# Kernel optimization log

Measured on AMD Instinct MI355X. Metric: run time of the kernel, lower is better.

## Reference

```python
import jax, jax.numpy as jnp
from jax import lax
import numpy as np


def _dw_xcorr_single(f, k):
    # f: (ch, Hf, Wf) search features; k: (ch, Hk, Wk) template kernel
    # Depthwise cross-correlation: one 2D correlation per channel.
    ch = f.shape[0]
    out = lax.conv_general_dilated(
        f[None],                 # (1, ch, Hf, Wf)
        k[:, None],              # (ch, 1, Hk, Wk) OIHW depthwise kernel
        window_strides=(1, 1),
        padding='VALID',
        dimension_numbers=('NCHW', 'OIHW', 'NCHW'),
        feature_group_count=ch,
    )
    return out[0]  # (ch, H, W)


def _conv3x3(x, w, b):
    # x: (N, C, H, W), w: (O, C, 3, 3), b: (O,)
    y = lax.conv_general_dilated(
        x, w, window_strides=(1, 1), padding='VALID',
        dimension_numbers=('NCHW', 'OIHW', 'NCHW'))
    return y + b[None, :, None, None]


def setup_inputs() -> dict:
    key = jax.random.key(0)
    k1, k2, k3, k4, k5, k6 = jax.random.split(key, 6)
    N, C = 128, 256
    x_f = jax.random.normal(k1, (N, C, 31, 31), dtype=jnp.float32)
    z_f = jax.random.normal(k2, (N, C, 7, 7), dtype=jnp.float32)
    # Conv params (Kaiming-uniform-like scale)
    s3 = 1.0 / np.sqrt(C * 9)
    heat_w = jax.random.uniform(k3, (1, C, 3, 3), jnp.float32, -s3, s3)
    heat_b = jax.random.uniform(k4, (1,), jnp.float32, -s3, s3)
    reg_w = jax.random.uniform(k5, (4, C, 3, 3), jnp.float32, -s3, s3)
    reg_b = jax.random.uniform(k6, (4,), jnp.float32, -s3, s3)
    return {"x_f": x_f, "z_f": z_f, "heat_w": heat_w, "heat_b": heat_b,
            "reg_w": reg_w, "reg_b": reg_b}


def reference(x_f, z_f, heat_w, heat_b, reg_w, reg_b):
    # Depthwise cross-correlation over batch (groups = N*ch in the original)
    corr = jax.vmap(_dw_xcorr_single)(x_f, z_f)  # (N, C, 25, 25)
    pred_heat = _conv3x3(corr, heat_w, heat_b)   # (N, 1, 23, 23)
    pred_reg = _conv3x3(corr, reg_w, reg_b)      # (N, 4, 23, 23)
    return (pred_heat, pred_reg)
```

## Files before the change

### kernel.cpp

```cpp
#include <hip/hip_runtime.h>

#define NB 128
#define NC 256
#define HX 31
#define WX 31
#define HC 25
#define WC 25
#define HO 23
#define WO 23
#define CHUNKS 8
#define CPB (NC / CHUNKS)
#define GRP 10
#define ZCH 56
#define WCH 48
#define CCH (HC * WC)

#define HEAT_SZ (NB * HO * WO)
#define REG_SZ  (NB * 4 * HO * WO)
#define OUT_TOTAL (HEAT_SZ + REG_SZ)

typedef float f4v __attribute__((ext_vector_type(4), aligned(4)));

__global__ void init_out_kernel(float* __restrict__ out,
                                const float* __restrict__ heat_b,
                                const float* __restrict__ reg_b) {
    int i = blockIdx.x * 256 + threadIdx.x;
    if (i >= OUT_TOTAL) return;
    if (i < HEAT_SZ) {
        out[i] = heat_b[0];
    } else {
        int j = i - HEAT_SZ;
        int o = (j / (HO * WO)) & 3;
        out[i] = reg_b[o];
    }
}

__launch_bounds__(256, 4)
__global__ void fused_head_kernel(const float* __restrict__ xf,
                                  const float* __restrict__ zf,
                                  const float* __restrict__ hw,
                                  const float* __restrict__ rw,
                                  float* __restrict__ out) {
    __shared__ __align__(16) float cs[GRP * CCH];
    __shared__ __align__(16) float zs[GRP * ZCH];
    __shared__ __align__(16) float ws[CPB * WCH];

    const int tid = threadIdx.x;
    const int n = blockIdx.x >> 3;
    const int chunk = blockIdx.x & 7;
    const int cbase = chunk * CPB;

    const int cl = tid / 25;
    const int tt = tid % 25;
    const int tr = tt / 5, tc = tt % 5;
    const int i0 = tr * 5, j0 = tc * 5;

    const int p0 = tid;
    const int p1 = tid + 256;
    const int p2 = tid + 512;
    const int oy0 = p0 / 23, ox0 = p0 - oy0 * 23;
    const int oy1 = p1 / 23, ox1 = p1 - oy1 * 23;
    const int oy2 = p2 / 23, ox2 = p2 - oy2 * 23;
    const int off0 = oy0 * WC + ox0;
    const int off1 = oy1 * WC + ox1;
    const int off2 = (tid < 17) ? (oy2 * WC + ox2) : 0;

    float accH0 = 0.f, accH1 = 0.f, accH2 = 0.f;
    float accR0[4] = {0.f, 0.f, 0.f, 0.f};
    float accR1[4] = {0.f, 0.f, 0.f, 0.f};
    float accR2[4] = {0.f, 0.f, 0.f, 0.f};

    const float* xn = xf + ((size_t)n * NC + cbase) * (HX * WX);
    const float* zn = zf + ((size_t)n * NC + cbase) * 49;

    for (int idx = tid; idx < CPB * 45; idx += 256) {
        int ch = idx / 45, j = idx - ch * 45;
        int c = cbase + ch;
        float v;
        if (j < 9) {
            v = hw[c * 9 + j];
        } else {
            int o = (j - 9) / 9;
            int jj = (j - 9) - o * 9;
            v = rw[((size_t)o * NC + c) * 9 + jj];
        }
        ws[ch * WCH + j] = v;
    }

    for (int g0 = 0; g0 < CPB; g0 += GRP) {
        const int G = (CPB - g0) < GRP ? (CPB - g0) : GRP;

        for (int idx = tid; idx < G * 49; idx += 256) {
            int ch = idx / 49, q = idx - ch * 49;
            int u = q / 7, v = q - u * 7;
            zs[ch * ZCH + u * 8 + v] = zn[(size_t)(g0 + ch) * 49 + q];
        }
        __syncthreads();

        if (cl < G) {
            const float* xb = xn + (size_t)(g0 + cl) * (HX * WX) + i0 * WX + j0;
            const float* zb = zs + cl * ZCH;

            float cacc[5][5];
            #pragma unroll
            for (int r = 0; r < 5; ++r)
                #pragma unroll
                for (int b = 0; b < 5; ++b) cacc[r][b] = 0.f;

            f4v c0 = *(const f4v*)(xb);
            f4v c1 = *(const f4v*)(xb + 4);
            f4v c2 = *(const f4v*)(xb + 7);

            #pragma unroll
            for (int rl = 0; rl < 11; ++rl) {
                f4v n0, n1, n2;
                if (rl < 10) {
                    const float* rp = xb + (rl + 1) * WX;
                    n0 = *(const f4v*)(rp);
                    n1 = *(const f4v*)(rp + 4);
                    n2 = *(const f4v*)(rp + 7);
                }
                const float xr[11] = {c0.x, c0.y, c0.z, c0.w,
                                      c1.x, c1.y, c1.z, c1.w,
                                      c2.y, c2.z, c2.w};
                #pragma unroll
                for (int u = 0; u < 7; ++u) {
                    const int r = rl - u;
                    if (r >= 0 && r < 5) {
                        f4v za = *(const f4v*)(zb + u * 8);
                        f4v zc = *(const f4v*)(zb + u * 8 + 4);
                        const float zz[7] = {za.x, za.y, za.z, za.w,
                                             zc.x, zc.y, zc.z};
                        #pragma unroll
                        for (int v = 0; v < 7; ++v)
                            #pragma unroll
                            for (int b = 0; b < 5; ++b)
                                cacc[r][b] = fmaf(zz[v], xr[b + v], cacc[r][b]);
                    }
                }
                if (rl < 10) { c0 = n0; c1 = n1; c2 = n2; }
            }
            float* cb = cs + cl * CCH + i0 * WC + j0;
            #pragma unroll
            for (int r = 0; r < 5; ++r)
                #pragma unroll
                for (int b = 0; b < 5; ++b) cb[r * WC + b] = cacc[r][b];
        }
        __syncthreads();

        for (int clc = 0; clc < G; ++clc) {
            float w[48];
            {
                const f4v* wp = (const f4v*)(ws + (size_t)(g0 + clc) * WCH);
                #pragma unroll
                for (int q = 0; q < 12; ++q) {
                    f4v t = wp[q];
                    w[q * 4 + 0] = t.x; w[q * 4 + 1] = t.y;
                    w[q * 4 + 2] = t.z; w[q * 4 + 3] = t.w;
                }
            }
            const float* cc = cs + clc * CCH;

            {
                const float* base = cc + off0;
                #pragma unroll
                for (int dy = 0; dy < 3; ++dy)
                    #pragma unroll
                    for (int dx = 0; dx < 3; ++dx) {
                        const float cv = base[dy * WC + dx];
                        const int k = dy * 3 + dx;
                        accH0    = fmaf(cv, w[k],      accH0);
                        accR0[0] = fmaf(cv, w[9 + k],  accR0[0]);
                        accR0[1] = fmaf(cv, w[18 + k], accR0[1]);
                        accR0[2] = fmaf(cv, w[27 + k], accR0[2]);
                        accR0[3] = fmaf(cv, w[36 + k], accR0[3]);
                    }
            }
            {
                const float* base = cc + off1;
                #pragma unroll
                for (int dy = 0; dy < 3; ++dy)
                    #pragma unroll
                    for (int dx = 0; dx < 3; ++dx) {
                        const float cv = base[dy * WC + dx];
                        const int k = dy * 3 + dx;
                        accH1    = fmaf(cv, w[k],      accH1);
                        accR1[0] = fmaf(cv, w[9 + k],  accR1[0]);
                        accR1[1] = fmaf(cv, w[18 + k], accR1[1]);
                        accR1[2] = fmaf(cv, w[27 + k], accR1[2]);
                        accR1[3] = fmaf(cv, w[36 + k], accR1[3]);
                    }
            }
            if (tid < 17) {
                const float* base = cc + off2;
                #pragma unroll
                for (int dy = 0; dy < 3; ++dy)
                    #pragma unroll
                    for (int dx = 0; dx < 3; ++dx) {
                        const float cv = base[dy * WC + dx];
                        const int k = dy * 3 + dx;
                        accH2    = fmaf(cv, w[k],      accH2);
                        accR2[0] = fmaf(cv, w[9 + k],  accR2[0]);
                        accR2[1] = fmaf(cv, w[18 + k], accR2[1]);
                        accR2[2] = fmaf(cv, w[27 + k], accR2[2]);
                        accR2[3] = fmaf(cv, w[36 + k], accR2[3]);
                    }
            }
        }
        __syncthreads();
    }

    float* outH = out + n * (HO * WO);
    float* outR = out + HEAT_SZ + (size_t)n * 4 * (HO * WO);

    atomicAdd(&outH[p0], accH0);
    #pragma unroll
    for (int o = 0; o < 4; ++o)
        atomicAdd(&outR[o * (HO * WO) + p0], accR0[o]);

    atomicAdd(&outH[p1], accH1);
    #pragma unroll
    for (int o = 0; o < 4; ++o)
        atomicAdd(&outR[o * (HO * WO) + p1], accR1[o]);

    if (tid < 17) {
        atomicAdd(&outH[p2], accH2);
        #pragma unroll
        for (int o = 0; o < 4; ++o)
            atomicAdd(&outR[o * (HO * WO) + p2], accR2[o]);
    }
}

extern "C" void kernel_launch(void* const* d_in, const int* in_sizes, int n_in,
                              void* d_out, int out_size, void* d_ws, size_t ws_size,
                              hipStream_t stream) {
    const float* x_f    = (const float*)d_in[0];
    const float* z_f    = (const float*)d_in[1];
    const float* heat_w = (const float*)d_in[2];
    const float* heat_b = (const float*)d_in[3];
    const float* reg_w  = (const float*)d_in[4];
    const float* reg_b  = (const float*)d_in[5];
    float* out = (float*)d_out;

    init_out_kernel<<<(OUT_TOTAL + 255) / 256, 256, 0, stream>>>(out, heat_b, reg_b);
    fused_head_kernel<<<NB * CHUNKS, 256, 0, stream>>>(x_f, z_f, heat_w, reg_w, out);
}
```

Baseline: 248.4 us.

## Store correlation tile as bf16 in LDS, split channels into 16 chunks

The intermediate correlation map in shared memory is now stored as bf16 (round-to-nearest-even) instead of fp32, roughly halving LDS usage per block. Channels are split across 16 chunks per image instead of 8, with groups of 8 channels and a fully unrolled group loop, and launch bounds request 8 blocks per CU. The aim is more blocks resident per CU and more parallelism. The cost is reduced precision in the correlation values feeding the 3x3 convolutions, twice as many atomic adds to the output, and more register pressure from the tighter launch bound.

Measured after the change: 752.0 us. 3.03x slower.

```diff
diff --git a/kernel.cpp b/kernel.cpp
--- a/kernel.cpp
+++ b/kernel.cpp
@@ -8,18 +8,30 @@
 #define WC 25
 #define HO 23
 #define WO 23
-#define CHUNKS 8
+#define CHUNKS 16
 #define CPB (NC / CHUNKS)
-#define GRP 10
+#define GRP 8
 #define ZCH 56
 #define WCH 48
-#define CCH (HC * WC)
+#define CCHS 640
 
 #define HEAT_SZ (NB * HO * WO)
 #define REG_SZ  (NB * 4 * HO * WO)
 #define OUT_TOTAL (HEAT_SZ + REG_SZ)
 
 typedef float f4v __attribute__((ext_vector_type(4), aligned(4)));
+
+__device__ __forceinline__ unsigned short f32_to_bf16_rtn(float f) {
+    union { float f; unsigned int u; } v; v.f = f;
+    unsigned int u = v.u;
+    u += 0x7FFFu + ((u >> 16) & 1u);
+    return (unsigned short)(u >> 16);
+}
+__device__ __forceinline__ float bf16_to_f32(unsigned short h) {
+    union { unsigned int u; float f; } v;
+    v.u = ((unsigned int)h) << 16;
+    return v.f;
+}
 
 __global__ void init_out_kernel(float* __restrict__ out,
                                 const float* __restrict__ heat_b,
@@ -35,19 +47,19 @@
     }
 }
 
-__launch_bounds__(256, 4)
+__launch_bounds__(256, 8)
 __global__ void fused_head_kernel(const float* __restrict__ xf,
                                   const float* __restrict__ zf,
                                   const float* __restrict__ hw,
                                   const float* __restrict__ rw,
                                   float* __restrict__ out) {
-    __shared__ __align__(16) float cs[GRP * CCH];
+    __shared__ __align__(16) unsigned short cs[GRP * CCHS];
     __shared__ __align__(16) float zs[GRP * ZCH];
     __shared__ __align__(16) float ws[CPB * WCH];
 
     const int tid = threadIdx.x;
-    const int n = blockIdx.x >> 3;
-    const int chunk = blockIdx.x & 7;
+    const int n = blockIdx.x >> 4;
+    const int chunk = blockIdx.x & 15;
     const int cbase = chunk * CPB;
 
     const int cl = tid / 25;
@@ -87,17 +99,17 @@
         ws[ch * WCH + j] = v;
     }
 
+    #pragma unroll
     for (int g0 = 0; g0 < CPB; g0 += GRP) {
-        const int G = (CPB - g0) < GRP ? (CPB - g0) : GRP;
-
-        for (int idx = tid; idx < G * 49; idx += 256) {
+
+        for (int idx = tid; idx < GRP * 49; idx += 256) {
             int ch = idx / 49, q = idx - ch * 49;
             int u = q / 7, v = q - u * 7;
             zs[ch * ZCH + u * 8 + v] = zn[(size_t)(g0 + ch) * 49 + q];
         }
         __syncthreads();
 
-        if (cl < G) {
+        if (cl < GRP) {
             const float* xb = xn + (size_t)(g0 + cl) * (HX * WX) + i0 * WX + j0;
             const float* zb = zs + cl * ZCH;
 
@@ -140,15 +152,16 @@
                 }
                 if (rl < 10) { c0 = n0; c1 = n1; c2 = n2; }
             }
-            float* cb = cs + cl * CCH + i0 * WC + j0;
+            unsigned short* cb = cs + cl * CCHS + i0 * WC + j0;
             #pragma unroll
             for (int r = 0; r < 5; ++r)
                 #pragma unroll
-                for (int b = 0; b < 5; ++b) cb[r * WC + b] = cacc[r][b];
+                for (int b = 0; b < 5; ++b)
+                    cb[r * WC + b] = f32_to_bf16_rtn(cacc[r][b]);
         }
         __syncthreads();
 
-        for (int clc = 0; clc < G; ++clc) {
+        for (int clc = 0; clc < GRP; ++clc) {
             float w[48];
             {
                 const f4v* wp = (const f4v*)(ws + (size_t)(g0 + clc) * WCH);
@@ -159,15 +172,15 @@
                     w[q * 4 + 2] = t.z; w[q * 4 + 3] = t.w;
                 }
             }
-            const float* cc = cs + clc * CCH;
+            const unsigned short* cc = cs + clc * CCHS;
 
             {
-                const float* base = cc + off0;
+                const unsigned short* base = cc + off0;
                 #pragma unroll
                 for (int dy = 0; dy < 3; ++dy)
                     #pragma unroll
                     for (int dx = 0; dx < 3; ++dx) {
-                        const float cv = base[dy * WC + dx];
+                        const float cv = bf16_to_f32(base[dy * WC + dx]);
                         const int k = dy * 3 + dx;
                         accH0    = fmaf(cv, w[k],      accH0);
                         accR0[0] = fmaf(cv, w[9 + k],  accR0[0]);
@@ -177,12 +190,12 @@
                     }
             }
             {
-                const float* base = cc + off1;
+                const unsigned short* base = cc + off1;
                 #pragma unroll
                 for (int dy = 0; dy < 3; ++dy)
                     #pragma unroll
                     for (int dx = 0; dx < 3; ++dx) {
-                        const float cv = base[dy * WC + dx];
+                        const float cv = bf16_to_f32(base[dy * WC + dx]);
                         const int k = dy * 3 + dx;
                         accH1    = fmaf(cv, w[k],      accH1);
                         accR1[0] = fmaf(cv, w[9 + k],  accR1[0]);
@@ -192,12 +205,12 @@
                     }
             }
             if (tid < 17) {
-                const float* base = cc + off2;
+                const unsigned short* base = cc + off2;
                 #pragma unroll
                 for (int dy = 0; dy < 3; ++dy)
                     #pragma unroll
                     for (int dx = 0; dx < 3; ++dx) {
-                        const float cv = base[dy * WC + dx];
+                        const float cv = bf16_to_f32(base[dy * WC + dx]);
                         const int k = dy * 3 + dx;
                         accH2    = fmaf(cv, w[k],      accH2);
                         accR2[0] = fmaf(cv, w[9 + k],  accR2[0]);
```
